# Kernel optimization log

Measured on AMD Instinct MI355X. Metric: run time of the kernel, lower is better.

The kernel has to match this reference:

```python
import jax, jax.numpy as jnp
import numpy as np

N, D, H, E_RAW = 100000, 128, 8, 1600000
C = D // H  # head dim = 16
NEG_SLOPE = 0.2
LN_EPS = 1e-5


def _glorot(key, shape):
    fan_in, fan_out = shape[0], shape[-1]
    lim = (6.0 / (fan_in + fan_out)) ** 0.5
    return jax.random.uniform(key, shape, jnp.float32, -lim, lim)


def setup_inputs() -> dict:
    key = jax.random.key(0)
    ks = jax.random.split(key, 16)
    inp = {
        "x": jax.random.normal(ks[0], (N, D), jnp.float32),
        "edge_index": jax.random.randint(ks[1], (2, E_RAW), 0, N, jnp.int64),
    }
    for l in range(2):
        o = 2 + 4 * l
        inp[f"Wl{l}"] = _glorot(ks[o + 0], (D, H * C))
        inp[f"Wr{l}"] = _glorot(ks[o + 1], (D, H * C))
        inp[f"att{l}"] = _glorot(ks[o + 2], (H, C))
        inp[f"b{l}"] = jnp.zeros((H * C,), jnp.float32)
        inp[f"g{l}"] = jnp.ones((D,), jnp.float32)
        inp[f"beta{l}"] = jnp.zeros((D,), jnp.float32)
    return inp


def _gatv2_layer(x, src, dst, Wl, Wr, att, b):
    # GATv2Conv: e_ij = att . leaky_relu(Wl x_j + Wr x_i); softmax over j -> i
    xl = (x @ Wl).reshape(N, H, C)  # source transform
    xr = (x @ Wr).reshape(N, H, C)  # target transform
    m = jax.nn.leaky_relu(xl[src] + xr[dst], NEG_SLOPE)  # [E,H,C]
    e = jnp.einsum("ehc,hc->eh", m, att)  # [E,H]
    emax = jax.ops.segment_max(e, dst, num_segments=N)[dst]
    ex = jnp.exp(e - emax)
    denom = jax.ops.segment_sum(ex, dst, num_segments=N)[dst]
    alpha = ex / denom  # per-destination softmax
    out = jax.ops.segment_sum(xl[src] * alpha[:, :, None], dst, num_segments=N)
    return out.reshape(N, H * C) + b


def _layernorm(x, g, beta):
    mu = jnp.mean(x, axis=-1, keepdims=True)
    var = jnp.var(x, axis=-1, keepdims=True)
    return (x - mu) * jax.lax.rsqrt(var + LN_EPS) * g + beta


def reference(x, edge_index, Wl0, Wr0, att0, b0, g0, beta0,
              Wl1, Wr1, att1, b1, g1, beta1):
    # add_self_loops=True (PyG default): every node attends to itself
    loop = jnp.arange(N, dtype=edge_index.dtype)
    src = jnp.concatenate([edge_index[0], loop])
    dst = jnp.concatenate([edge_index[1], loop])
    params = [(Wl0, Wr0, att0, b0, g0, beta0), (Wl1, Wr1, att1, b1, g1, beta1)]
    for Wl, Wr, att, b, g, beta in params:
        residual = x
        h = _gatv2_layer(x, src, dst, Wl, Wr, att, b)  # dropout is identity (eval)
        h = jax.nn.elu(h)
        x = _layernorm(h + residual, g, beta)
    return x
```

## Files before the change

kernel.cpp:

```cpp
#include <hip/hip_runtime.h>
#include <cstdint>

#define LEAKY 0.2f
#define LN_EPS 1e-5f

typedef __attribute__((ext_vector_type(8))) short short8;
typedef __attribute__((ext_vector_type(4))) float f32x4;
typedef __attribute__((ext_vector_type(2))) float f32x2;

__device__ __forceinline__ ushort bf16_rne(float x) {
    unsigned u = __float_as_uint(x);
    unsigned r = (u + 0x7fffu + ((u >> 16) & 1u)) >> 16;
    return (ushort)r;
}
__device__ __forceinline__ float bf16_to_f(ushort h) {
    return __uint_as_float(((unsigned)h) << 16);
}
__device__ __forceinline__ f32x2 unpk(uint u) {
    f32x2 r;
    r.x = __uint_as_float(u << 16);
    r.y = __uint_as_float(u & 0xffff0000u);
    return r;
}
__device__ __forceinline__ uint cvt_pk_bf16(float lo, float hi) {
    uint r;
    asm("v_cvt_pk_bf16_f32 %0, %1, %2" : "=v"(r) : "v"(lo), "v"(hi));
    return r;
}
template <int CTRL>
__device__ __forceinline__ float dpp_radd(float v) {
    int sh = __builtin_amdgcn_update_dpp(0, __float_as_int(v), CTRL, 0xF, 0xF, true);
    return v + __int_as_float(sh);
}

__global__ void hist_part(const int* __restrict__ ei, int er, int etot, int n,
                          int* __restrict__ deg) {
    const int xcd = blockIdx.x & 7;
    const int lo = (int)((long long)n * xcd >> 3);
    const int hi = (int)((long long)n * (xcd + 1) >> 3);
    const int stride = (gridDim.x >> 3) * blockDim.x;
    for (int e = (blockIdx.x >> 3) * blockDim.x + threadIdx.x; e < etot;
         e += stride) {
        int dst = (e < er) ? ei[er + e] : (e - er);
        if (dst >= lo && dst < hi) atomicAdd(&deg[dst], 1);
    }
}

__global__ void fill_part(const int* __restrict__ ei, int er, int etot, int n,
                          int* __restrict__ woff, int* __restrict__ colv) {
    const int xcd = blockIdx.x & 7;
    const int lo = (int)((long long)n * xcd >> 3);
    const int hi = (int)((long long)n * (xcd + 1) >> 3);
    const int stride = (gridDim.x >> 3) * blockDim.x;
    for (int e = (blockIdx.x >> 3) * blockDim.x + threadIdx.x; e < etot;
         e += stride) {
        int dst = (e < er) ? ei[er + e] : (e - er);
        if (dst >= lo && dst < hi) {
            int src = (e < er) ? ei[e] : dst;
            int pos = atomicAdd(&woff[dst], 1);
            colv[pos] = src;
        }
    }
}

__global__ __launch_bounds__(1024) void scanA(const int* __restrict__ deg,
                                              int* __restrict__ escan,
                                              int* __restrict__ bsum, int n) {
    __shared__ int wsum[16], wpre[16];
    const int lane = threadIdx.x & 63, wv = threadIdx.x >> 6;
    const int i = blockIdx.x * 1024 + threadIdx.x;
    int v = (i < n) ? deg[i] : 0;
    int x = v;
#pragma unroll
    for (int off = 1; off < 64; off <<= 1) {
        int y = __shfl_up(x, off, 64);
        if (lane >= off) x += y;
    }
    if (lane == 63) wsum[wv] = x;
    __syncthreads();
    if (wv == 0) {
        int s = (lane < 16) ? wsum[lane] : 0;
#pragma unroll
        for (int off = 1; off < 16; off <<= 1) {
            int y = __shfl_up(s, off, 64);
            if (lane >= off) s += y;
        }
        if (lane < 16) wpre[lane] = s;
    }
    __syncthreads();
    int excl = x - v + (wv ? wpre[wv - 1] : 0);
    if (i < n) escan[i] = excl;
    if (threadIdx.x == 1023) bsum[blockIdx.x] = wpre[15];
}

__global__ __launch_bounds__(1024) void scanB(const int* __restrict__ bsum,
                                              int* __restrict__ bpre, int nb,
                                              int* __restrict__ offs, int n) {
    __shared__ int wsum[16], wpre[16];
    const int lane = threadIdx.x & 63, wv = threadIdx.x >> 6;
    const int i = threadIdx.x;
    int v = (i < nb) ? bsum[i] : 0;
    int x = v;
#pragma unroll
    for (int off = 1; off < 64; off <<= 1) {
        int y = __shfl_up(x, off, 64);
        if (lane >= off) x += y;
    }
    if (lane == 63) wsum[wv] = x;
    __syncthreads();
    if (wv == 0) {
        int s = (lane < 16) ? wsum[lane] : 0;
#pragma unroll
        for (int off = 1; off < 16; off <<= 1) {
            int y = __shfl_up(s, off, 64);
            if (lane >= off) s += y;
        }
        if (lane < 16) wpre[lane] = s;
    }
    __syncthreads();
    if (i < nb) bpre[i] = x - v + (wv ? wpre[wv - 1] : 0);
    if (threadIdx.x == 1023) offs[n] = wpre[15];
}

__global__ void scanC(const int* __restrict__ escan, const int* __restrict__ bpre,
                      int* __restrict__ offs, int* __restrict__ woff, int n) {
    int i = blockIdx.x * 256 + threadIdx.x;
    if (i >= n) return;
    int o = escan[i] + bpre[i >> 10];
    offs[i] = o;
    woff[i] = o;
}

__global__ void cvt_w2(const float* __restrict__ Wl0, const float* __restrict__ Wr0,
                       const float* __restrict__ Wl1, const float* __restrict__ Wr1,
                       ushort* __restrict__ Whi, ushort* __restrict__ Wlo) {
    int t = blockIdx.x * 256 + threadIdx.x;
    int layer = t >> 15;
    int i = t & 32767;
    int colblk = i >> 11;
    int ks = (i >> 9) & 3;
    int lane = (i >> 3) & 63;
    int j = i & 7;
    int col = colblk * 16 + (lane & 15);
    int k = ks * 32 + (lane >> 4) * 8 + j;
    const float* Wl = layer ? Wl1 : Wl0;
    const float* Wr = layer ? Wr1 : Wr0;
    float v = (col < 128) ? Wl[(size_t)k * 128 + col]
                          : Wr[(size_t)k * 128 + (col - 128)];
    ushort h = bf16_rne(v);
    Whi[t] = h;
    Wlo[t] = bf16_rne(v - bf16_to_f(h));
}

template <bool ABF16>
__global__ __launch_bounds__(256) void gemm_mfma(
    const void* __restrict__ Xin,
    const ushort* __restrict__ Wfhi, const ushort* __restrict__ Wflo,
    uint* __restrict__ Olb, uint* __restrict__ Orb, int nrows) {
    __shared__ float4 xs[64 * 32];
    const int t = threadIdx.x;
    const int wave = t >> 6, lane = t & 63;
    const int m0 = blockIdx.x * 64;
    if (ABF16) {
        const uint4* Xv = (const uint4*)Xin + (size_t)m0 * 16;
        uint4* xsb = (uint4*)xs;
#pragma unroll
        for (int i = 0; i < 4; ++i) {
            int idx = i * 256 + t;
            int row = idx >> 4, kc = idx & 15;
            uint4 v = {0u, 0u, 0u, 0u};
            if (m0 + row < nrows) v = Xv[idx];
            xsb[row * 16 + (kc ^ (row & 7))] = v;
        }
    } else {
        const float4* Xv = (const float4*)Xin + (size_t)m0 * 32;
#pragma unroll
        for (int i = 0; i < 8; ++i) {
            int idx = i * 256 + t;
            int row = idx >> 5, kc = idx & 31;
            float4 v = {0.f, 0.f, 0.f, 0.f};
            if (m0 + row < nrows) v = Xv[idx];
            xs[row * 32 + (kc ^ (row & 7))] = v;
        }
    }
    __syncthreads();

    const int lrow = lane & 15;
    const int lkc = (lane >> 4) * 2;
    f32x4 acc[4][4];
#pragma unroll
    for (int mt = 0; mt < 4; ++mt)
#pragma unroll
        for (int nt = 0; nt < 4; ++nt) acc[mt][nt] = (f32x4){0.f, 0.f, 0.f, 0.f};

#pragma unroll 1
    for (int ks = 0; ks < 4; ++ks) {
        short8 ahi[4];
#pragma unroll
        for (int mt = 0; mt < 4; ++mt) {
            const int row = mt * 16 + lrow;
            if (ABF16) {
                const int slot = ks * 4 + (lane >> 4);
                uint4 w = ((const uint4*)xs)[row * 16 + (slot ^ (row & 7))];
                ahi[mt] = *(const short8*)&w;
            } else {
                const int kc0 = ks * 8 + lkc;
                float4 v0 = xs[row * 32 + (kc0 ^ (row & 7))];
                float4 v1 = xs[row * 32 + ((kc0 + 1) ^ (row & 7))];
                uint4 q;
                q.x = cvt_pk_bf16(v0.x, v0.y);
                q.y = cvt_pk_bf16(v0.z, v0.w);
                q.z = cvt_pk_bf16(v1.x, v1.y);
                q.w = cvt_pk_bf16(v1.z, v1.w);
                ahi[mt] = *(const short8*)&q;
            }
        }
#pragma unroll
        for (int nt = 0; nt < 4; ++nt) {
            size_t off = (((size_t)(wave * 4 + nt) * 4 + ks) * 64 + lane) * 8;
            short8 bhi = *(const short8*)&Wfhi[off];
            short8 blo = *(const short8*)&Wflo[off];
#pragma unroll
            for (int mt = 0; mt < 4; ++mt) {
                acc[mt][nt] = __builtin_amdgcn_mfma_f32_16x16x32_bf16(
                    ahi[mt], blo, acc[mt][nt], 0, 0, 0);
                acc[mt][nt] = __builtin_amdgcn_mfma_f32_16x16x32_bf16(
                    ahi[mt], bhi, acc[mt][nt], 0, 0, 0);
            }
        }
    }
    uint* __restrict__ O = (wave < 2) ? Olb : Orb;
    const int cbase = (wave * 64) & 127;
    const int crow0 = (lane >> 4) * 4;
    const bool evn = (lane & 1) == 0;
#pragma unroll
    for (int mt = 0; mt < 4; ++mt) {
#pragma unroll
        for (int i = 0; i < 4; ++i) {
            const int row = m0 + mt * 16 + crow0 + i;
#pragma unroll
            for (int nt = 0; nt < 4; ++nt) {
                float val = acc[mt][nt][i];
                float pv = __shfl_xor(val, 1);
                uint pk = (uint)bf16_rne(val) | ((uint)bf16_rne(pv) << 16);
                if (evn && row < nrows) {
                    const int col = cbase + nt * 16 + lrow;
                    O[(size_t)row * 64 + (col >> 1)] = pk;
                }
            }
        }
    }
}

template <bool RBF16, bool OBF16>
__global__ __launch_bounds__(256) void gat_agg(
    const uint* __restrict__ xl, const uint* __restrict__ xr,
    const int* __restrict__ offs, const int* __restrict__ colv,
    const float* __restrict__ att,
    const float* __restrict__ bias, const float* __restrict__ gamma,
    const float* __restrict__ beta, const void* __restrict__ resid,
    void* __restrict__ out, int nnode) {
    const int lane = threadIdx.x & 63;
    const int wid = __builtin_amdgcn_readfirstlane(threadIdx.x >> 6);
    const int wave0 = blockIdx.x * 4 + wid;
    const int wstride = gridDim.x * 4;
    const f32x2 att2 = ((const f32x2*)att)[lane];
    const f32x2 b2 = ((const f32x2*)bias)[lane];
    const f32x2 g2 = ((const f32x2*)gamma)[lane];
    const f32x2 be2 = ((const f32x2*)beta)[lane];
    for (int gid = wave0; gid < nnode; gid += wstride) {
        const uint xru = __builtin_nontemporal_load(xr + (size_t)gid * 64 + lane);
        const f32x2 xr2 = unpk(xru);
        float den = 0.f;
        f32x2 acc = {0.f, 0.f};
        int e = offs[gid];
        const int e1 = offs[gid + 1];
        for (; e + 4 <= e1; e += 4) {
            int s[4];
#pragma unroll
            for (int k = 0; k < 4; ++k)
                s[k] = __builtin_amdgcn_readfirstlane(colv[e + k]);
            uint u[4];
#pragma unroll
            for (int k = 0; k < 4; ++k) u[k] = xl[(size_t)s[k] * 64 + lane];
#pragma unroll
            for (int k = 0; k < 4; ++k) {
                f32x2 a = unpk(u[k]);
                f32x2 m = a + xr2;
                f32x2 l = m * LEAKY;
                m.x = fmaxf(m.x, l.x); m.y = fmaxf(m.y, l.y);
                f32x2 t = m * att2;
                float p = t.x + t.y;
                p = dpp_radd<0xB1>(p);
                p = dpp_radd<0x4E>(p);
                p = dpp_radd<0x141>(p);
                float ex = __expf(p);
                den += ex;
                acc += a * ex;
            }
        }
        for (; e < e1; ++e) {
            int s0 = __builtin_amdgcn_readfirstlane(colv[e]);
            uint u0 = xl[(size_t)s0 * 64 + lane];
            f32x2 a0 = unpk(u0);
            f32x2 m0 = a0 + xr2;
            f32x2 l0 = m0 * LEAKY;
            m0.x = fmaxf(m0.x, l0.x); m0.y = fmaxf(m0.y, l0.y);
            f32x2 t0 = m0 * att2;
            float p0 = t0.x + t0.y;
            p0 = dpp_radd<0xB1>(p0);
            p0 = dpp_radd<0x4E>(p0);
            p0 = dpp_radd<0x141>(p0);
            float ex0 = __expf(p0);
            den += ex0;
            acc += a0 * ex0;
        }
        const float inv_den = 1.f / den;
        f32x2 v = acc * inv_den + b2;
        v.x = v.x > 0.f ? v.x : expm1f(v.x);
        v.y = v.y > 0.f ? v.y : expm1f(v.y);
        f32x2 r2;
        if (RBF16) {
            uint ru = __builtin_nontemporal_load(
                (const uint*)resid + (size_t)gid * 64 + lane);
            r2 = unpk(ru);
        } else {
            r2 = __builtin_nontemporal_load(
                (const f32x2*)resid + (size_t)gid * 64 + lane);
        }
        f32x2 tv = v + r2;
        float s = tv.x + tv.y, ss = tv.x * tv.x + tv.y * tv.y;
        s = dpp_radd<0xB1>(s);   ss = dpp_radd<0xB1>(ss);
        s = dpp_radd<0x4E>(s);   ss = dpp_radd<0x4E>(ss);
        s = dpp_radd<0x141>(s);  ss = dpp_radd<0x141>(ss);
        s = dpp_radd<0x140>(s);  ss = dpp_radd<0x140>(ss);
        s += __shfl_xor(s, 16);  ss += __shfl_xor(ss, 16);
        s += __shfl_xor(s, 32);  ss += __shfl_xor(ss, 32);
        const float mu = s * 0.0078125f;
        const float var = ss * 0.0078125f - mu * mu;
        const float iv = rsqrtf(var + LN_EPS);
        f32x2 o = (tv - mu) * iv * g2 + be2;
        if (OBF16) {
            uint po = (uint)bf16_rne(o.x) | ((uint)bf16_rne(o.y) << 16);
            __builtin_nontemporal_store(po, (uint*)out + (size_t)gid * 64 + lane);
        } else {
            __builtin_nontemporal_store(o, (f32x2*)out + (size_t)gid * 64 + lane);
        }
    }
}

extern "C" void kernel_launch(void* const* d_in, const int* in_sizes, int n_in,
                              void* d_out, int out_size, void* d_ws, size_t ws_size,
                              hipStream_t stream) {
    const float* x   = (const float*)d_in[0];
    const int*   ei  = (const int*)d_in[1];
    const float* Wl0 = (const float*)d_in[2];
    const float* Wr0 = (const float*)d_in[3];
    const float* at0 = (const float*)d_in[4];
    const float* b0  = (const float*)d_in[5];
    const float* g0  = (const float*)d_in[6];
    const float* be0 = (const float*)d_in[7];
    const float* Wl1 = (const float*)d_in[8];
    const float* Wr1 = (const float*)d_in[9];
    const float* at1 = (const float*)d_in[10];
    const float* b1  = (const float*)d_in[11];
    const float* g1  = (const float*)d_in[12];
    const float* be1 = (const float*)d_in[13];

    const int NF = in_sizes[0];
    const int n  = NF / 128;
    const int er = in_sizes[1] / 2;
    const int etot = er + n;
    const int nb = (n + 1023) / 1024;

    uint* A     = (uint*)d_ws;
    uint* B     = A + (size_t)NF / 2;
    uint* C1    = B + (size_t)NF / 2;
    ushort* Whi = (ushort*)(C1 + (size_t)NF / 2);
    ushort* Wlo = Whi + 65536;
    int* deg    = (int*)(Wlo + 65536);
    int* woff   = deg + n;
    int* offs   = woff + n;
    int* escan  = offs + (n + 4);
    int* bsum   = escan + n;
    int* bpre   = bsum + 1024;
    int* colv   = bpre + 1024;
    float* C    = (float*)d_out;

    (void)hipMemsetAsync(deg, 0, (size_t)n * sizeof(int), stream);
    hist_part<<<2048, 256, 0, stream>>>(ei, er, etot, n, deg);
    scanA<<<nb, 1024, 0, stream>>>(deg, escan, bsum, n);
    scanB<<<1, 1024, 0, stream>>>(bsum, bpre, nb, offs, n);
    scanC<<<(n + 255) / 256, 256, 0, stream>>>(escan, bpre, offs, woff, n);
    fill_part<<<2048, 256, 0, stream>>>(ei, er, etot, n, woff, colv);
    cvt_w2<<<256, 256, 0, stream>>>(Wl0, Wr0, Wl1, Wr1, Whi, Wlo);

    const int gblk = (n + 63) / 64;

    gemm_mfma<false><<<gblk, 256, 0, stream>>>(x, Whi, Wlo, A, B, n);
    gat_agg<false, true><<<2048, 256, 0, stream>>>(
        A, B, offs, colv, at0, b0, g0, be0, x, C1, n);
    gemm_mfma<true><<<gblk, 256, 0, stream>>>(C1, Whi + 32768, Wlo + 32768,
                                              A, B, n);
    gat_agg<true, false><<<2048, 256, 0, stream>>>(
        A, B, offs, colv, at1, b1, g1, be1, C1, C, n);
}
```

Measured before the change: 448.5 us.

## Software-pipeline neighbor gathers in GAT aggregation and hoist weight loads in GEMM

The edge aggregation loop now prefetches the next four source indices and xl rows while computing the current four. Out-of-range edges are clamped to the last valid edge and masked by zeroing their exp weight, which removes the scalar tail loop. In the projection GEMM, all B-fragment loads for a k-step are issued before the MFMA loop so their latency can overlap. The cost is more live registers and some redundant gathers on the final partial and prefetch iterations.

```diff
diff --git a/kernel.cpp b/kernel.cpp
--- a/kernel.cpp
+++ b/kernel.cpp
@@ -195,6 +195,13 @@
 
 #pragma unroll 1
     for (int ks = 0; ks < 4; ++ks) {
+        short8 bhi[4], blo[4];
+#pragma unroll
+        for (int nt = 0; nt < 4; ++nt) {
+            size_t off = (((size_t)(wave * 4 + nt) * 4 + ks) * 64 + lane) * 8;
+            bhi[nt] = *(const short8*)&Wfhi[off];
+            blo[nt] = *(const short8*)&Wflo[off];
+        }
         short8 ahi[4];
 #pragma unroll
         for (int mt = 0; mt < 4; ++mt) {
@@ -217,15 +224,12 @@
         }
 #pragma unroll
         for (int nt = 0; nt < 4; ++nt) {
-            size_t off = (((size_t)(wave * 4 + nt) * 4 + ks) * 64 + lane) * 8;
-            short8 bhi = *(const short8*)&Wfhi[off];
-            short8 blo = *(const short8*)&Wflo[off];
 #pragma unroll
             for (int mt = 0; mt < 4; ++mt) {
                 acc[mt][nt] = __builtin_amdgcn_mfma_f32_16x16x32_bf16(
-                    ahi[mt], blo, acc[mt][nt], 0, 0, 0);
+                    ahi[mt], blo[nt], acc[mt][nt], 0, 0, 0);
                 acc[mt][nt] = __builtin_amdgcn_mfma_f32_16x16x32_bf16(
-                    ahi[mt], bhi, acc[mt][nt], 0, 0, 0);
+                    ahi[mt], bhi[nt], acc[mt][nt], 0, 0, 0);
             }
         }
     }
@@ -273,47 +277,47 @@
         const f32x2 xr2 = unpk(xru);
         float den = 0.f;
         f32x2 acc = {0.f, 0.f};
-        int e = offs[gid];
+        const int e0 = offs[gid];
         const int e1 = offs[gid + 1];
-        for (; e + 4 <= e1; e += 4) {
-            int s[4];
-#pragma unroll
-            for (int k = 0; k < 4; ++k)
-                s[k] = __builtin_amdgcn_readfirstlane(colv[e + k]);
-            uint u[4];
-#pragma unroll
-            for (int k = 0; k < 4; ++k) u[k] = xl[(size_t)s[k] * 64 + lane];
+        const int e1m = e1 - 1;
+        const int niter = (e1 - e0 + 3) >> 2;
+        int s0 = __builtin_amdgcn_readfirstlane(colv[min(e0 + 0, e1m)]);
+        int s1 = __builtin_amdgcn_readfirstlane(colv[min(e0 + 1, e1m)]);
+        int s2 = __builtin_amdgcn_readfirstlane(colv[min(e0 + 2, e1m)]);
+        int s3 = __builtin_amdgcn_readfirstlane(colv[min(e0 + 3, e1m)]);
+        uint u0 = xl[(size_t)s0 * 64 + lane];
+        uint u1 = xl[(size_t)s1 * 64 + lane];
+        uint u2 = xl[(size_t)s2 * 64 + lane];
+        uint u3 = xl[(size_t)s3 * 64 + lane];
+        int ebase = e0;
+        for (int it = 0; it < niter; ++it) {
+            const int en = ebase + 4;
+            int t0i = __builtin_amdgcn_readfirstlane(colv[min(en + 0, e1m)]);
+            int t1i = __builtin_amdgcn_readfirstlane(colv[min(en + 1, e1m)]);
+            int t2i = __builtin_amdgcn_readfirstlane(colv[min(en + 2, e1m)]);
+            int t3i = __builtin_amdgcn_readfirstlane(colv[min(en + 3, e1m)]);
+            uint v0 = xl[(size_t)t0i * 64 + lane];
+            uint v1 = xl[(size_t)t1i * 64 + lane];
+            uint v2 = xl[(size_t)t2i * 64 + lane];
+            uint v3 = xl[(size_t)t3i * 64 + lane];
+            uint uu[4] = {u0, u1, u2, u3};
 #pragma unroll
             for (int k = 0; k < 4; ++k) {
-                f32x2 a = unpk(u[k]);
+                f32x2 a = unpk(uu[k]);
                 f32x2 m = a + xr2;
                 f32x2 l = m * LEAKY;
                 m.x = fmaxf(m.x, l.x); m.y = fmaxf(m.y, l.y);
-                f32x2 t = m * att2;
-                float p = t.x + t.y;
+                f32x2 tt = m * att2;
+                float p = tt.x + tt.y;
                 p = dpp_radd<0xB1>(p);
                 p = dpp_radd<0x4E>(p);
                 p = dpp_radd<0x141>(p);
-                float ex = __expf(p);
+                float ex = (ebase + k < e1) ? __expf(p) : 0.f;
                 den += ex;
                 acc += a * ex;
             }
-        }
-        for (; e < e1; ++e) {
-            int s0 = __builtin_amdgcn_readfirstlane(colv[e]);
-            uint u0 = xl[(size_t)s0 * 64 + lane];
-            f32x2 a0 = unpk(u0);
-            f32x2 m0 = a0 + xr2;
-            f32x2 l0 = m0 * LEAKY;
-            m0.x = fmaxf(m0.x, l0.x); m0.y = fmaxf(m0.y, l0.y);
-            f32x2 t0 = m0 * att2;
-            float p0 = t0.x + t0.y;
-            p0 = dpp_radd<0xB1>(p0);
-            p0 = dpp_radd<0x4E>(p0);
-            p0 = dpp_radd<0x141>(p0);
-            float ex0 = __expf(p0);
-            den += ex0;
-            acc += a0 * ex0;
+            u0 = v0; u1 = v1; u2 = v2; u3 = v3;
+            ebase = en;
         }
         const float inv_den = 1.f / den;
         f32x2 v = acc * inv_den + b2;
```

Result: slower. 458.8 us (+2.3%).
